# Optimization experiments

Hardware: AMD Instinct MI355X
Metric: run time of the kernel (lower is better)

The kernel has to match this reference:

```python
import jax, jax.numpy as jnp
import numpy as np

B, N, S = 8, 4096, 1024
D1, D2 = 128, 256
IN_CH, OUT_CH = D1 + D2, 256
BN_EPS = 1e-5


def setup_inputs() -> dict:
    key = jax.random.key(0)
    ks = jax.random.split(key, 12)
    inp = {
        "xyz1": jax.random.normal(ks[0], (B, N, 3), jnp.float32),
        "xyz2": jax.random.normal(ks[1], (B, S, 3), jnp.float32),
        "points1": jax.random.normal(ks[2], (B, N, D1), jnp.float32),
        "points2": jax.random.normal(ks[3], (B, S, D2), jnp.float32),
        # fuse: Conv1d(in_ch->out_ch, k=1) + BN
        "W_fuse": jax.random.normal(ks[4], (OUT_CH, IN_CH), jnp.float32) * (1.0 / np.sqrt(IN_CH)),
        "b_fuse": jnp.zeros((OUT_CH,), jnp.float32),
        "g_fuse": jnp.ones((OUT_CH,), jnp.float32),
        "bt_fuse": jnp.zeros((OUT_CH,), jnp.float32),
        # res block net1: Conv1d(out_ch->out_ch) + BN (res_expansion=1.0)
        "W1": jax.random.normal(ks[5], (OUT_CH, OUT_CH), jnp.float32) * (1.0 / np.sqrt(OUT_CH)),
        "b1": jnp.zeros((OUT_CH,), jnp.float32),
        "g1": jnp.ones((OUT_CH,), jnp.float32),
        "bt1": jnp.zeros((OUT_CH,), jnp.float32),
        # res block net2: Conv1d(out_ch->out_ch) + BN
        "W2": jax.random.normal(ks[6], (OUT_CH, OUT_CH), jnp.float32) * (1.0 / np.sqrt(OUT_CH)),
        "b2": jnp.zeros((OUT_CH,), jnp.float32),
        "g2": jnp.ones((OUT_CH,), jnp.float32),
        "bt2": jnp.zeros((OUT_CH,), jnp.float32),
    }
    return inp


def _bn(x, g, b):
    # BatchNorm1d training-mode forward: stats over (batch, length), x: [B, C, L]
    m = jnp.mean(x, axis=(0, 2), keepdims=True)
    v = jnp.var(x, axis=(0, 2), keepdims=True)
    return (x - m) * jax.lax.rsqrt(v + BN_EPS) * g[None, :, None] + b[None, :, None]


def _conv1x1(x, W, b):
    # x: [B, C_in, L], W: [C_out, C_in] -> [B, C_out, L]
    return jnp.einsum("oc,bcl->bol", W, x) + b[None, :, None]


def _gelu(x):
    return jax.nn.gelu(x, approximate=False)  # torch nn.GELU default (erf)


def reference(xyz1, xyz2, points1, points2,
              W_fuse, b_fuse, g_fuse, bt_fuse,
              W1, b1, g1, bt1, W2, b2, g2, bt2):
    # squared pairwise distances [B, N, S] without B x N x S x 3 intermediate
    d = (jnp.sum(xyz1 * xyz1, -1)[:, :, None]
         - 2.0 * jnp.einsum("bnc,bsc->bns", xyz1, xyz2)
         + jnp.sum(xyz2 * xyz2, -1)[:, None, :])
    # 3 nearest coarse points per dense point (== sort ascending, take first 3)
    neg_d3, idx = jax.lax.top_k(-d, 3)            # [B, N, 3]
    d3 = -neg_d3
    recip = 1.0 / (d3 + 1e-8)
    w = recip / jnp.sum(recip, axis=2, keepdims=True)  # [B, N, 3]
    gathered = points2[jnp.arange(points2.shape[0])[:, None, None], idx]  # [B, N, 3, D2]
    interp = jnp.sum(gathered * w[..., None], axis=2)  # [B, N, D2]

    new_points = jnp.concatenate([points1, interp], axis=-1)  # [B, N, D1+D2]
    x = jnp.transpose(new_points, (0, 2, 1))                   # [B, C, N]

    # fuse: conv-bn-gelu
    x = _gelu(_bn(_conv1x1(x, W_fuse, b_fuse), g_fuse, bt_fuse))
    # residual block: gelu(bn(conv(gelu(bn(conv(x))))) + x)
    y = _gelu(_bn(_conv1x1(x, W1, b1), g1, bt1))
    y = _bn(_conv1x1(y, W2, b2), g2, bt2)
    x = _gelu(y + x)

    return jnp.transpose(x, (0, 2, 1))  # [B, N, out_ch]
```

## Files before the change

### kernel.cpp

```cpp
#include <hip/hip_runtime.h>
#include <hip/hip_bf16.h>

constexpr int Bb = 8, Nn = 4096, Ss = 1024;
constexpr int D1 = 128, D2 = 256, KIN = 384, OC = 256;
constexpr int L = Bb * Nn;
constexpr float BN_EPS = 1e-5f;

typedef __attribute__((ext_vector_type(4))) float floatx4;
typedef __attribute__((ext_vector_type(8))) __bf16 bf16x8;

#define DEV __device__ __forceinline__

DEV float bf2f(unsigned short u) {
    union { unsigned int i; float f; } v; v.i = ((unsigned int)u) << 16; return v.f;
}
DEV unsigned short f2bf(float f) {
    union { float f; unsigned int i; } v; v.f = f;
    unsigned int x = v.i;
    return (unsigned short)((x + 0x7FFFu + ((x >> 16) & 1u)) >> 16);
}
DEV float gelu_f(float x) {
    float u = x * (0.7978845608f + 0.0356774081f * x * x);
    float t = __expf(-2.0f * u);
    return x * __builtin_amdgcn_rcpf(1.0f + t);
}

DEV bool probe_isf(const unsigned int* __restrict__ w, int tid) {
    unsigned int lo = w[tid & 63] & 0xFFFFu;
    int e = (int)((lo >> 7) & 0xFF);
    unsigned long long m = __ballot(e >= 100 && e <= 144);
    return __popcll(m) < 48;
}

template <int K> DEV int permoff(int off) {
    int row = off / K, rr = off - row * K;
    int cg = (rr >> 3) & 7;
    return row * K + (rr & ~63) + (((cg ^ (row & 7)) << 3)) + (rr & 7);
}

DEV void merge3(float& d0, float& d1, float& d2, int& i0, int& i1, int& i2,
                float e0, float e1, float e2, int j0, int j1, int j2, bool pref) {
    float a0 = d0, a1 = d1, a2 = d2; int x0 = i0, x1 = i1, x2 = i2;
    float b0 = e0, b1 = e1;          int y0 = j0, y1 = j1;
    bool t = pref ? (a0 <= b0) : (a0 < b0);
    d0 = t ? a0 : b0; i0 = t ? x0 : y0;
    a0 = t ? a1 : a0; x0 = t ? x1 : x0;
    a1 = t ? a2 : a1; x1 = t ? x2 : x1;
    b0 = t ? b0 : b1; y0 = t ? y0 : y1;
    b1 = t ? b1 : e2; y1 = t ? y1 : j2;
    t = pref ? (a0 <= b0) : (a0 < b0);
    d1 = t ? a0 : b0; i1 = t ? x0 : y0;
    a0 = t ? a1 : a0; x0 = t ? x1 : x0;
    b0 = t ? b0 : b1; y0 = t ? y0 : y1;
    t = pref ? (a0 <= b0) : (a0 < b0);
    d2 = t ? a0 : b0; i2 = t ? x0 : y0;
}

__global__ __launch_bounds__(256) void k_front(const void* __restrict__ xyz1_,
                                               const void* __restrict__ xyz2_,
                                               const void* __restrict__ w0_,
                                               const void* __restrict__ w1_,
                                               const void* __restrict__ w2_,
                                               unsigned short* __restrict__ Wdst,
                                               float* __restrict__ stats,
                                               int* __restrict__ dflag,
                                               int* __restrict__ nn_idx,
                                               float* __restrict__ nn_w) {
    int tid = threadIdx.x;
    int bid = blockIdx.x;
    bool isf = probe_isf((const unsigned int*)xyz1_, tid);

    if (bid < 6) {
        stats[bid * 256 + tid] = 0.0f;
        if (bid == 0 && tid == 0) *dflag = isf ? 1 : 0;
        return;
    }
    if (bid < 902) {
        int i = (bid - 6) * 256 + tid;
        const void* src; int off;
        if (i < 98304)       { src = w0_; off = permoff<384>(i); }
        else if (i < 163840) { src = w1_; off = permoff<256>(i - 98304); }
        else                 { src = w2_; off = permoff<256>(i - 163840); }
        Wdst[i] = isf ? f2bf(((const float*)src)[off]) : ((const unsigned short*)src)[off];
        return;
    }

    __shared__ alignas(16) float s4[Ss * 4 + 32];
    int bn0 = (bid - 902) * 32;
    int b = bn0 >> 12;

    if (isf) {
        const float* p2 = (const float*)xyz2_ + (size_t)b * Ss * 3;
        for (int i = tid; i < Ss * 3; i += 256) {
            int s = i / 3, k = i - s * 3;
            s4[s * 4 + k + ((s >> 7) << 2)] = p2[i];
        }
    } else {
        const unsigned short* p2 = (const unsigned short*)xyz2_ + (size_t)b * Ss * 3;
        for (int i = tid; i < Ss * 3; i += 256) {
            int s = i / 3, k = i - s * 3;
            s4[s * 4 + k + ((s >> 7) << 2)] = bf2f(p2[i]);
        }
    }
    __syncthreads();
    for (int s = tid; s < Ss; s += 256) {
        int a = s * 4 + ((s >> 7) << 2);
        float x = s4[a], y = s4[a + 1], z = s4[a + 2];
        s4[a + 3] = x * x + y * y + z * z;
    }
    __syncthreads();

    int part = tid & 7;
    int bn = bn0 + (tid >> 3);
    float x1, y1, z1;
    if (isf) {
        const float* p1 = (const float*)xyz1_ + (size_t)bn * 3;
        x1 = p1[0]; y1 = p1[1]; z1 = p1[2];
    } else {
        const unsigned short* p1 = (const unsigned short*)xyz1_ + (size_t)bn * 3;
        x1 = bf2f(p1[0]); y1 = bf2f(p1[1]); z1 = bf2f(p1[2]);
    }
    float n1 = x1 * x1 + y1 * y1 + z1 * z1;

    float d0 = 3.4e38f, d1 = 3.4e38f, d2 = 3.4e38f;
    int i0 = 0, i1 = 0, i2 = 0;
    const float* sp = &s4[part * 516];
#pragma unroll 4
    for (int j = 0; j < 128; ++j) {
        float4 qv = *(const float4*)(sp + j * 4);
        float d = n1 + qv.w - 2.0f * (x1 * qv.x + y1 * qv.y + z1 * qv.z);
        int s = part * 128 + j;
        bool c2 = d < d2, c1 = d < d1, c0 = d < d0;
        d2 = c1 ? d1 : (c2 ? d : d2); i2 = c1 ? i1 : (c2 ? s : i2);
        d1 = c0 ? d0 : (c1 ? d : d1); i1 = c0 ? i0 : (c1 ? s : i1);
        d0 = c0 ? d  : d0;            i0 = c0 ? s  : i0;
    }
#pragma unroll
    for (int m = 1; m <= 4; m <<= 1) {
        float e0 = __shfl_xor(d0, m, 64), e1 = __shfl_xor(d1, m, 64), e2 = __shfl_xor(d2, m, 64);
        int   j0 = __shfl_xor(i0, m, 64), j1 = __shfl_xor(i1, m, 64), j2 = __shfl_xor(i2, m, 64);
        bool pref = (part < (part ^ m));
        merge3(d0, d1, d2, i0, i1, i2, e0, e1, e2, j0, j1, j2, pref);
    }
    if (part == 0) {
        float r0 = 1.0f / (d0 + 1e-8f), r1 = 1.0f / (d1 + 1e-8f), r2 = 1.0f / (d2 + 1e-8f);
        float rs = 1.0f / (r0 + r1 + r2);
        nn_idx[bn * 3 + 0] = i0; nn_idx[bn * 3 + 1] = i1; nn_idx[bn * 3 + 2] = i2;
        nn_w[bn * 3 + 0] = r0 * rs; nn_w[bn * 3 + 1] = r1 * rs; nn_w[bn * 3 + 2] = r2 * rs;
    }
}

__global__ __launch_bounds__(256) void k_gemm1(const void* __restrict__ p1_,
                                               const void* __restrict__ p2_,
                                               const int* __restrict__ nn_idx,
                                               const float* __restrict__ nn_w,
                                               const int* __restrict__ dflag,
                                               const unsigned short* __restrict__ W,
                                               unsigned short* __restrict__ Out,
                                               float* __restrict__ S1, float* __restrict__ S2) {
    __shared__ alignas(16) unsigned short As[64 * 64];
    __shared__ alignas(16) unsigned short Bs[256 * 64];
    __shared__ float sS1[256], sS2[256];

    int tid = threadIdx.x;
    int l0 = blockIdx.x * 64;
    int wn = tid >> 6, lane = tid & 63, quad = lane >> 4, lr = lane & 15;
    bool isf = (*dflag != 0);

    floatx4 acc[4][4];
#pragma unroll
    for (int mi = 0; mi < 4; ++mi)
#pragma unroll
        for (int ni = 0; ni < 4; ++ni) acc[mi][ni] = (floatx4){0.f, 0.f, 0.f, 0.f};

    for (int kc = 0; kc < KIN / 64; ++kc) {
        __syncthreads();
#pragma unroll
        for (int it = 0; it < 8; ++it) {
            int chunk = it * 4 + wn;
            int row = chunk * 8 + (lane >> 3);
            int cg = lane & 7;
            const unsigned short* src = W + (size_t)row * KIN + kc * 64 + cg * 8;
            __builtin_amdgcn_global_load_lds(
                (const __attribute__((address_space(1))) void*)src,
                (__attribute__((address_space(3))) void*)&Bs[chunk * 512],
                16, 0, 0);
        }
#pragma unroll
        for (int it = 0; it < 2; ++it) {
            int idx = it * 256 + tid, row = idx >> 3, c8 = idx & 7;
            int pt = l0 + row;
            int c0 = kc * 64 + c8 * 8;
            union { uint4 v; unsigned short u[8]; } va;
            if (c0 < D1) {
                if (isf) {
                    const float* p = (const float*)p1_ + (size_t)pt * D1 + c0;
                    float4 f0 = *(const float4*)p;
                    float4 f1 = *(const float4*)(p + 4);
                    va.u[0] = f2bf(f0.x); va.u[1] = f2bf(f0.y); va.u[2] = f2bf(f0.z); va.u[3] = f2bf(f0.w);
                    va.u[4] = f2bf(f1.x); va.u[5] = f2bf(f1.y); va.u[6] = f2bf(f1.z); va.u[7] = f2bf(f1.w);
                } else {
                    va.v = *(const uint4*)((const unsigned short*)p1_ + (size_t)pt * D1 + c0);
                }
            } else {
                int c2 = c0 - D1;
                int b = pt >> 12;
                int j0 = nn_idx[pt * 3], j1 = nn_idx[pt * 3 + 1], j2 = nn_idx[pt * 3 + 2];
                float w0 = nn_w[pt * 3], w1 = nn_w[pt * 3 + 1], w2 = nn_w[pt * 3 + 2];
                if (isf) {
                    const float* base = (const float*)p2_;
                    const float* r0 = base + ((size_t)(b * Ss + j0)) * D2 + c2;
                    const float* r1 = base + ((size_t)(b * Ss + j1)) * D2 + c2;
                    const float* r2 = base + ((size_t)(b * Ss + j2)) * D2 + c2;
#pragma unroll
                    for (int h = 0; h < 2; ++h) {
                        float4 a0 = *(const float4*)(r0 + h * 4);
                        float4 a1 = *(const float4*)(r1 + h * 4);
                        float4 a2 = *(const float4*)(r2 + h * 4);
                        va.u[h * 4 + 0] = f2bf(w0 * a0.x + w1 * a1.x + w2 * a2.x);
                        va.u[h * 4 + 1] = f2bf(w0 * a0.y + w1 * a1.y + w2 * a2.y);
                        va.u[h * 4 + 2] = f2bf(w0 * a0.z + w1 * a1.z + w2 * a2.z);
                        va.u[h * 4 + 3] = f2bf(w0 * a0.w + w1 * a1.w + w2 * a2.w);
                    }
                } else {
                    const unsigned short* base = (const unsigned short*)p2_;
                    uint4 v0 = *(const uint4*)(base + ((size_t)(b * Ss + j0)) * D2 + c2);
                    uint4 v1 = *(const uint4*)(base + ((size_t)(b * Ss + j1)) * D2 + c2);
                    uint4 v2 = *(const uint4*)(base + ((size_t)(b * Ss + j2)) * D2 + c2);
                    const unsigned short* u0 = (const unsigned short*)&v0;
                    const unsigned short* u1 = (const unsigned short*)&v1;
                    const unsigned short* u2 = (const unsigned short*)&v2;
#pragma unroll
                    for (int j = 0; j < 8; ++j)
                        va.u[j] = f2bf(w0 * bf2f(u0[j]) + w1 * bf2f(u1[j]) + w2 * bf2f(u2[j]));
                }
            }
            *(uint4*)&As[row * 64 + ((c8 ^ (row & 7)) << 3)] = va.v;
        }
        __syncthreads();
#pragma unroll
        for (int ks8 = 0; ks8 < 2; ++ks8) {
            bf16x8 af[4], bfr[4];
#pragma unroll
            for (int mi = 0; mi < 4; ++mi) {
                int ra = mi * 16 + lr;
                af[mi] = *(const bf16x8*)&As[ra * 64 + ((((ks8 << 2) + quad) ^ (ra & 7)) << 3)];
            }
#pragma unroll
            for (int ni = 0; ni < 4; ++ni) {
                int rb = wn * 64 + ni * 16 + lr;
                bfr[ni] = *(const bf16x8*)&Bs[rb * 64 + ((((ks8 << 2) + quad) ^ (rb & 7)) << 3)];
            }
#pragma unroll
            for (int mi = 0; mi < 4; ++mi)
#pragma unroll
                for (int ni = 0; ni < 4; ++ni)
                    acc[mi][ni] = __builtin_amdgcn_mfma_f32_16x16x32_bf16(af[mi], bfr[ni], acc[mi][ni], 0, 0, 0);
        }
    }

    float p1a[4] = {0, 0, 0, 0}, p2a[4] = {0, 0, 0, 0};
#pragma unroll
    for (int mi = 0; mi < 4; ++mi)
#pragma unroll
        for (int ni = 0; ni < 4; ++ni)
#pragma unroll
            for (int r = 0; r < 4; ++r) {
                float v = acc[mi][ni][r];
                int row = l0 + mi * 16 + quad * 4 + r;
                int col = wn * 64 + ni * 16 + lr;
                Out[(size_t)row * OC + col] = f2bf(v);
                p1a[ni] += v; p2a[ni] += v * v;
            }
    sS1[tid] = 0.f; sS2[tid] = 0.f;
    __syncthreads();
#pragma unroll
    for (int ni = 0; ni < 4; ++ni) {
        atomicAdd(&sS1[wn * 64 + ni * 16 + lr], p1a[ni]);
        atomicAdd(&sS2[wn * 64 + ni * 16 + lr], p2a[ni]);
    }
    __syncthreads();
    atomicAdd(&S1[tid], sS1[tid]);
    atomicAdd(&S2[tid], sS2[tid]);
}

template <int K>
__global__ __launch_bounds__(256) void k_gemm(const unsigned short* __restrict__ A,
                                              const unsigned short* __restrict__ W,
                                              unsigned short* __restrict__ Out,
                                              float* __restrict__ S1, float* __restrict__ S2,
                                              const float* __restrict__ S1in,
                                              const float* __restrict__ S2in,
                                              const void* __restrict__ g_,
                                              const void* __restrict__ bt_,
                                              const int* __restrict__ dflag) {
    __shared__ alignas(16) unsigned short As[64 * K];
    __shared__ alignas(16) unsigned short Bs[256 * 64];
    __shared__ float sS1[256], sS2[256];
    __shared__ float sCA[256], sCC[256];

    int tid = threadIdx.x;
    int l0 = blockIdx.x * 64;
    int wn = tid >> 6, lane = tid & 63, quad = lane >> 4, lr = lane & 15;

    {
        float m = S1in[tid] * (1.0f / (float)L);
        float var = S2in[tid] * (1.0f / (float)L) - m * m;
        float g, bt;
        if (*dflag) { g = ((const float*)g_)[tid]; bt = ((const float*)bt_)[tid]; }
        else { g = bf2f(((const unsigned short*)g_)[tid]); bt = bf2f(((const unsigned short*)bt_)[tid]); }
        float a = g * rsqrtf(var + BN_EPS);
        sCA[tid] = a;
        sCC[tid] = bt - m * a;
    }
    __syncthreads();

#pragma unroll
    for (int it = 0; it < (64 * K / 8) / 256; ++it) {
        int idx = it * 256 + tid;
        int row = idx >> 5, cg = idx & 31;
        union { uint4 v; unsigned short u[8]; } va;
        va.v = *(const uint4*)(A + (size_t)(l0 + row) * K + cg * 8);
        int kb = cg * 8;
#pragma unroll
        for (int j = 0; j < 8; ++j) {
            float f = bf2f(va.u[j]);
            va.u[j] = f2bf(gelu_f(sCA[kb + j] * f + sCC[kb + j]));
        }
        int sg = (cg & 24) | ((cg & 7) ^ (row & 7));
        *(uint4*)&As[row * K + sg * 8] = va.v;
    }

    floatx4 acc[4][4];
#pragma unroll
    for (int mi = 0; mi < 4; ++mi)
#pragma unroll
        for (int ni = 0; ni < 4; ++ni) acc[mi][ni] = (floatx4){0.f, 0.f, 0.f, 0.f};

    constexpr int KC = K / 64;
    for (int kc = 0; kc < KC; ++kc) {
        __syncthreads();
#pragma unroll
        for (int it = 0; it < 8; ++it) {
            int chunk = it * 4 + wn;
            int row = chunk * 8 + (lane >> 3);
            int cg = lane & 7;
            const unsigned short* src = W + (size_t)row * K + kc * 64 + cg * 8;
            __builtin_amdgcn_global_load_lds(
                (const __attribute__((address_space(1))) void*)src,
                (__attribute__((address_space(3))) void*)&Bs[chunk * 512],
                16, 0, 0);
        }
        __syncthreads();
#pragma unroll
        for (int ks8 = 0; ks8 < 2; ++ks8) {
            bf16x8 af[4], bfr[4];
#pragma unroll
            for (int mi = 0; mi < 4; ++mi) {
                int ra = mi * 16 + lr;
                int g = kc * 8 + ((((ks8 << 2) + quad)) ^ (ra & 7));
                af[mi] = *(const bf16x8*)&As[ra * K + g * 8];
            }
#pragma unroll
            for (int ni = 0; ni < 4; ++ni) {
                int rb = wn * 64 + ni * 16 + lr;
                bfr[ni] = *(const bf16x8*)&Bs[rb * 64 + ((((ks8 << 2) + quad) ^ (rb & 7)) << 3)];
            }
#pragma unroll
            for (int mi = 0; mi < 4; ++mi)
#pragma unroll
                for (int ni = 0; ni < 4; ++ni)
                    acc[mi][ni] = __builtin_amdgcn_mfma_f32_16x16x32_bf16(af[mi], bfr[ni], acc[mi][ni], 0, 0, 0);
        }
    }

    float p1a[4] = {0, 0, 0, 0}, p2a[4] = {0, 0, 0, 0};
#pragma unroll
    for (int mi = 0; mi < 4; ++mi)
#pragma unroll
        for (int ni = 0; ni < 4; ++ni)
#pragma unroll
            for (int r = 0; r < 4; ++r) {
                float v = acc[mi][ni][r];
                int row = l0 + mi * 16 + quad * 4 + r;
                int col = wn * 64 + ni * 16 + lr;
                Out[(size_t)row * OC + col] = f2bf(v);
                p1a[ni] += v; p2a[ni] += v * v;
            }
    sS1[tid] = 0.f; sS2[tid] = 0.f;
    __syncthreads();
#pragma unroll
    for (int ni = 0; ni < 4; ++ni) {
        atomicAdd(&sS1[wn * 64 + ni * 16 + lr], p1a[ni]);
        atomicAdd(&sS2[wn * 64 + ni * 16 + lr], p2a[ni]);
    }
    __syncthreads();
    atomicAdd(&S1[tid], sS1[tid]);
    atomicAdd(&S2[tid], sS2[tid]);
}

__global__ __launch_bounds__(256) void k_final(const unsigned short* __restrict__ t0,
                                               const unsigned short* __restrict__ t2,
                                               const float* __restrict__ S1_0, const float* __restrict__ S2_0,
                                               const float* __restrict__ S1_2, const float* __restrict__ S2_2,
                                               const void* __restrict__ g0_, const void* __restrict__ bt0_,
                                               const void* __restrict__ g2_, const void* __restrict__ bt2_,
                                               const int* __restrict__ dflag,
                                               void* __restrict__ out_) {
    __shared__ float sA0[256], sC0[256], sA2[256], sC2[256];
    int tid = threadIdx.x;
    bool isf = (*dflag != 0);
    {
        float m0 = S1_0[tid] * (1.0f / (float)L);
        float v0_ = S2_0[tid] * (1.0f / (float)L) - m0 * m0;
        float m2 = S1_2[tid] * (1.0f / (float)L);
        float v2_ = S2_2[tid] * (1.0f / (float)L) - m2 * m2;
        float g0, b0, g2, b2;
        if (isf) {
            g0 = ((const float*)g0_)[tid]; b0 = ((const float*)bt0_)[tid];
            g2 = ((const float*)g2_)[tid]; b2 = ((const float*)bt2_)[tid];
        } else {
            g0 = bf2f(((const unsigned short*)g0_)[tid]); b0 = bf2f(((const unsigned short*)bt0_)[tid]);
            g2 = bf2f(((const unsigned short*)g2_)[tid]); b2 = bf2f(((const unsigned short*)bt2_)[tid]);
        }
        float a0 = g0 * rsqrtf(v0_ + BN_EPS);
        float a2 = g2 * rsqrtf(v2_ + BN_EPS);
        sA0[tid] = a0; sC0[tid] = b0 - m0 * a0;
        sA2[tid] = a2; sC2[tid] = b2 - m2 * a2;
    }
    __syncthreads();

    int idx = (blockIdx.x * 256 + tid) * 8;
    int col = idx & (OC - 1);
    union { uint4 v; unsigned short u[8]; } v0, v2;
    v0.v = *(const uint4*)(t0 + idx);
    v2.v = *(const uint4*)(t2 + idx);
    float r[8];
#pragma unroll
    for (int j = 0; j < 8; ++j) {
        float x = gelu_f(sA0[col + j] * bf2f(v0.u[j]) + sC0[col + j]);
        float y = sA2[col + j] * bf2f(v2.u[j]) + sC2[col + j];
        r[j] = gelu_f(x + y);
    }
    if (isf) {
        float* o = (float*)out_ + idx;
        float4 lo = {r[0], r[1], r[2], r[3]};
        float4 hi = {r[4], r[5], r[6], r[7]};
        *(float4*)o = lo;
        *(float4*)(o + 4) = hi;
    } else {
        union { uint4 v; unsigned short u[8]; } vo;
#pragma unroll
        for (int j = 0; j < 8; ++j) vo.u[j] = f2bf(r[j]);
        *(uint4*)((unsigned short*)out_ + idx) = vo.v;
    }
}

extern "C" void kernel_launch(void* const* d_in, const int* in_sizes, int n_in,
                              void* d_out, int out_size, void* d_ws, size_t ws_size,
                              hipStream_t stream) {
    const void* xyz1    = d_in[0];
    const void* xyz2    = d_in[1];
    const void* points1 = d_in[2];
    const void* points2 = d_in[3];
    const void* W_fuse  = d_in[4];
    const void* g_fuse  = d_in[6];
    const void* bt_fuse = d_in[7];
    const void* W1      = d_in[8];
    const void* g1      = d_in[10];
    const void* bt1     = d_in[11];
    const void* W2      = d_in[12];
    const void* g2      = d_in[14];
    const void* bt2     = d_in[15];

    char* ws = (char*)d_ws;
    unsigned short* t2 = (unsigned short*)ws;
    unsigned short* t0 = (unsigned short*)(ws + 25165824);
    unsigned short* t1 = (unsigned short*)d_out;
    int*   nn_idx = (int*)(ws + 41943040);
    float* nn_w   = (float*)(ws + 42336256);
    float* stats  = (float*)(ws + 42729472);
    int*   dflag  = (int*)(ws + 42729472 + 3072 * 4);
    unsigned short* Wbf = (unsigned short*)(ws + 42745856);

    float *S1_0 = stats,        *S2_0 = stats + 256;
    float *S1_1 = stats + 512,  *S2_1 = stats + 768;
    float *S1_2 = stats + 1024, *S2_2 = stats + 1280;

    k_front<<<1926, 256, 0, stream>>>(xyz1, xyz2, W_fuse, W1, W2, Wbf, stats, dflag, nn_idx, nn_w);
    k_gemm1<<<L / 64, 256, 0, stream>>>(points1, points2, nn_idx, nn_w, dflag,
                                        Wbf, t0, S1_0, S2_0);
    k_gemm<OC><<<L / 64, 256, 0, stream>>>(t0, Wbf + 98304, t1, S1_1, S2_1,
                                           S1_0, S2_0, g_fuse, bt_fuse, dflag);
    k_gemm<OC><<<L / 64, 256, 0, stream>>>(t1, Wbf + 163840, t2, S1_2, S2_2,
                                           S1_1, S2_1, g1, bt1, dflag);
    k_final<<<L * OC / (256 * 8), 256, 0, stream>>>(t0, t2, S1_0, S2_0, S1_2, S2_2,
                                                    g_fuse, bt_fuse, g2, bt2, dflag, d_out);
}
```

Before: 229.1 us.

## Shrink GEMM block tiles to raise occupancy and grid size

The fuse GEMM now uses a 32-row tile instead of 64, and the residual GEMMs split the output channels into two 128-column halves with 64 rows each. Both kernels get launch_bounds with a minimum of 4 blocks per unit. The residual GEMM no longer preloads the whole 64x256 A panel with GELU-BN applied into LDS. It now loads and transforms one 64-wide K chunk per iteration, which cuts LDS use and lets more blocks be resident. The cost is more W reloads per output, and in the residual GEMMs each A chunk's GELU is computed twice, once per column half.

After: 235.6 us. 1.03x slower.

```diff
diff --git a/kernel.cpp b/kernel.cpp
--- a/kernel.cpp
+++ b/kernel.cpp
@@ -34,8 +34,8 @@
 
 template <int K> DEV int permoff(int off) {
     int row = off / K, rr = off - row * K;
-    int cg = (rr >> 3) & 7;
-    return row * K + (rr & ~63) + (((cg ^ (row & 7)) << 3)) + (rr & 7);
+    int cg_ = (rr >> 3) & 7;
+    return row * K + (rr & ~63) + (((cg_ ^ (row & 7)) << 3)) + (rr & 7);
 }
 
 DEV void merge3(float& d0, float& d1, float& d2, int& i0, int& i1, int& i2,
@@ -150,26 +150,26 @@
     }
 }
 
-__global__ __launch_bounds__(256) void k_gemm1(const void* __restrict__ p1_,
-                                               const void* __restrict__ p2_,
-                                               const int* __restrict__ nn_idx,
-                                               const float* __restrict__ nn_w,
-                                               const int* __restrict__ dflag,
-                                               const unsigned short* __restrict__ W,
-                                               unsigned short* __restrict__ Out,
-                                               float* __restrict__ S1, float* __restrict__ S2) {
-    __shared__ alignas(16) unsigned short As[64 * 64];
+__global__ __launch_bounds__(256, 4) void k_gemm1(const void* __restrict__ p1_,
+                                                  const void* __restrict__ p2_,
+                                                  const int* __restrict__ nn_idx,
+                                                  const float* __restrict__ nn_w,
+                                                  const int* __restrict__ dflag,
+                                                  const unsigned short* __restrict__ W,
+                                                  unsigned short* __restrict__ Out,
+                                                  float* __restrict__ S1, float* __restrict__ S2) {
+    __shared__ alignas(16) unsigned short As[32 * 64];
     __shared__ alignas(16) unsigned short Bs[256 * 64];
     __shared__ float sS1[256], sS2[256];
 
     int tid = threadIdx.x;
-    int l0 = blockIdx.x * 64;
+    int l0 = blockIdx.x * 32;
     int wn = tid >> 6, lane = tid & 63, quad = lane >> 4, lr = lane & 15;
     bool isf = (*dflag != 0);
 
-    floatx4 acc[4][4];
-#pragma unroll
-    for (int mi = 0; mi < 4; ++mi)
+    floatx4 acc[2][4];
+#pragma unroll
+    for (int mi = 0; mi < 2; ++mi)
 #pragma unroll
         for (int ni = 0; ni < 4; ++ni) acc[mi][ni] = (floatx4){0.f, 0.f, 0.f, 0.f};
 
@@ -179,16 +179,15 @@
         for (int it = 0; it < 8; ++it) {
             int chunk = it * 4 + wn;
             int row = chunk * 8 + (lane >> 3);
-            int cg = lane & 7;
-            const unsigned short* src = W + (size_t)row * KIN + kc * 64 + cg * 8;
+            int cg_ = lane & 7;
+            const unsigned short* src = W + (size_t)row * KIN + kc * 64 + cg_ * 8;
             __builtin_amdgcn_global_load_lds(
                 (const __attribute__((address_space(1))) void*)src,
                 (__attribute__((address_space(3))) void*)&Bs[chunk * 512],
                 16, 0, 0);
         }
-#pragma unroll
-        for (int it = 0; it < 2; ++it) {
-            int idx = it * 256 + tid, row = idx >> 3, c8 = idx & 7;
+        {
+            int row = tid >> 3, c8 = tid & 7;
             int pt = l0 + row;
             int c0 = kc * 64 + c8 * 8;
             union { uint4 v; unsigned short u[8]; } va;
@@ -240,9 +239,9 @@
         __syncthreads();
 #pragma unroll
         for (int ks8 = 0; ks8 < 2; ++ks8) {
-            bf16x8 af[4], bfr[4];
-#pragma unroll
-            for (int mi = 0; mi < 4; ++mi) {
+            bf16x8 af[2], bfr[4];
+#pragma unroll
+            for (int mi = 0; mi < 2; ++mi) {
                 int ra = mi * 16 + lr;
                 af[mi] = *(const bf16x8*)&As[ra * 64 + ((((ks8 << 2) + quad) ^ (ra & 7)) << 3)];
             }
@@ -252,7 +251,7 @@
                 bfr[ni] = *(const bf16x8*)&Bs[rb * 64 + ((((ks8 << 2) + quad) ^ (rb & 7)) << 3)];
             }
 #pragma unroll
-            for (int mi = 0; mi < 4; ++mi)
+            for (int mi = 0; mi < 2; ++mi)
 #pragma unroll
                 for (int ni = 0; ni < 4; ++ni)
                     acc[mi][ni] = __builtin_amdgcn_mfma_f32_16x16x32_bf16(af[mi], bfr[ni], acc[mi][ni], 0, 0, 0);
@@ -261,7 +260,7 @@
 
     float p1a[4] = {0, 0, 0, 0}, p2a[4] = {0, 0, 0, 0};
 #pragma unroll
-    for (int mi = 0; mi < 4; ++mi)
+    for (int mi = 0; mi < 2; ++mi)
 #pragma unroll
         for (int ni = 0; ni < 4; ++ni)
 #pragma unroll
@@ -284,24 +283,25 @@
     atomicAdd(&S2[tid], sS2[tid]);
 }
 
-template <int K>
-__global__ __launch_bounds__(256) void k_gemm(const unsigned short* __restrict__ A,
-                                              const unsigned short* __restrict__ W,
-                                              unsigned short* __restrict__ Out,
-                                              float* __restrict__ S1, float* __restrict__ S2,
-                                              const float* __restrict__ S1in,
-                                              const float* __restrict__ S2in,
-                                              const void* __restrict__ g_,
-                                              const void* __restrict__ bt_,
-                                              const int* __restrict__ dflag) {
-    __shared__ alignas(16) unsigned short As[64 * K];
-    __shared__ alignas(16) unsigned short Bs[256 * 64];
-    __shared__ float sS1[256], sS2[256];
+__global__ __launch_bounds__(256, 4) void k_gemm(const unsigned short* __restrict__ A,
+                                                 const unsigned short* __restrict__ W,
+                                                 unsigned short* __restrict__ Out,
+                                                 float* __restrict__ S1, float* __restrict__ S2,
+                                                 const float* __restrict__ S1in,
+                                                 const float* __restrict__ S2in,
+                                                 const void* __restrict__ g_,
+                                                 const void* __restrict__ bt_,
+                                                 const int* __restrict__ dflag) {
+    __shared__ alignas(16) unsigned short As[64 * 64];
+    __shared__ alignas(16) unsigned short Bs[128 * 64];
+    __shared__ float sS1[128], sS2[128];
     __shared__ float sCA[256], sCC[256];
 
     int tid = threadIdx.x;
-    int l0 = blockIdx.x * 64;
+    int l0 = (blockIdx.x >> 1) * 64;
+    int n0 = (blockIdx.x & 1) * 128;
     int wn = tid >> 6, lane = tid & 63, quad = lane >> 4, lr = lane & 15;
+    int wr = wn >> 1, wc = wn & 1;
 
     {
         float m = S1in[tid] * (1.0f / (float)L);
@@ -312,62 +312,57 @@
         float a = g * rsqrtf(var + BN_EPS);
         sCA[tid] = a;
         sCC[tid] = bt - m * a;
-    }
-    __syncthreads();
-
-#pragma unroll
-    for (int it = 0; it < (64 * K / 8) / 256; ++it) {
-        int idx = it * 256 + tid;
-        int row = idx >> 5, cg = idx & 31;
-        union { uint4 v; unsigned short u[8]; } va;
-        va.v = *(const uint4*)(A + (size_t)(l0 + row) * K + cg * 8);
-        int kb = cg * 8;
-#pragma unroll
-        for (int j = 0; j < 8; ++j) {
-            float f = bf2f(va.u[j]);
-            va.u[j] = f2bf(gelu_f(sCA[kb + j] * f + sCC[kb + j]));
-        }
-        int sg = (cg & 24) | ((cg & 7) ^ (row & 7));
-        *(uint4*)&As[row * K + sg * 8] = va.v;
-    }
-
-    floatx4 acc[4][4];
-#pragma unroll
-    for (int mi = 0; mi < 4; ++mi)
+        if (tid < 128) { sS1[tid] = 0.f; sS2[tid] = 0.f; }
+    }
+
+    floatx4 acc[2][4];
+#pragma unroll
+    for (int mi = 0; mi < 2; ++mi)
 #pragma unroll
         for (int ni = 0; ni < 4; ++ni) acc[mi][ni] = (floatx4){0.f, 0.f, 0.f, 0.f};
 
-    constexpr int KC = K / 64;
-    for (int kc = 0; kc < KC; ++kc) {
+    for (int kc = 0; kc < OC / 64; ++kc) {
         __syncthreads();
 #pragma unroll
-        for (int it = 0; it < 8; ++it) {
+        for (int it = 0; it < 4; ++it) {
             int chunk = it * 4 + wn;
             int row = chunk * 8 + (lane >> 3);
-            int cg = lane & 7;
-            const unsigned short* src = W + (size_t)row * K + kc * 64 + cg * 8;
+            int cg_ = lane & 7;
+            const unsigned short* src = W + (size_t)(n0 + row) * OC + kc * 64 + cg_ * 8;
             __builtin_amdgcn_global_load_lds(
                 (const __attribute__((address_space(1))) void*)src,
                 (__attribute__((address_space(3))) void*)&Bs[chunk * 512],
                 16, 0, 0);
         }
+#pragma unroll
+        for (int it = 0; it < 2; ++it) {
+            int idx = it * 256 + tid, row = idx >> 3, c8 = idx & 7;
+            union { uint4 v; unsigned short u[8]; } va;
+            va.v = *(const uint4*)(A + (size_t)(l0 + row) * OC + kc * 64 + c8 * 8);
+            int kb = kc * 64 + c8 * 8;
+#pragma unroll
+            for (int j = 0; j < 8; ++j) {
+                float f = bf2f(va.u[j]);
+                va.u[j] = f2bf(gelu_f(sCA[kb + j] * f + sCC[kb + j]));
+            }
+            *(uint4*)&As[row * 64 + ((c8 ^ (row & 7)) << 3)] = va.v;
+        }
         __syncthreads();
 #pragma unroll
         for (int ks8 = 0; ks8 < 2; ++ks8) {
-            bf16x8 af[4], bfr[4];
-#pragma unroll
-            for (int mi = 0; mi < 4; ++mi) {
-                int ra = mi * 16 + lr;
-                int g = kc * 8 + ((((ks8 << 2) + quad)) ^ (ra & 7));
-                af[mi] = *(const bf16x8*)&As[ra * K + g * 8];
+            bf16x8 af[2], bfr[4];
+#pragma unroll
+            for (int mi = 0; mi < 2; ++mi) {
+                int ra = wr * 32 + mi * 16 + lr;
+                af[mi] = *(const bf16x8*)&As[ra * 64 + ((((ks8 << 2) + quad) ^ (ra & 7)) << 3)];
             }
 #pragma unroll
             for (int ni = 0; ni < 4; ++ni) {
-                int rb = wn * 64 + ni * 16 + lr;
+                int rb = wc * 64 + ni * 16 + lr;
                 bfr[ni] = *(const bf16x8*)&Bs[rb * 64 + ((((ks8 << 2) + quad) ^ (rb & 7)) << 3)];
             }
 #pragma unroll
-            for (int mi = 0; mi < 4; ++mi)
+            for (int mi = 0; mi < 2; ++mi)
 #pragma unroll
                 for (int ni = 0; ni < 4; ++ni)
                     acc[mi][ni] = __builtin_amdgcn_mfma_f32_16x16x32_bf16(af[mi], bfr[ni], acc[mi][ni], 0, 0, 0);
@@ -376,27 +371,28 @@
 
     float p1a[4] = {0, 0, 0, 0}, p2a[4] = {0, 0, 0, 0};
 #pragma unroll
-    for (int mi = 0; mi < 4; ++mi)
+    for (int mi = 0; mi < 2; ++mi)
 #pragma unroll
         for (int ni = 0; ni < 4; ++ni)
 #pragma unroll
             for (int r = 0; r < 4; ++r) {
                 float v = acc[mi][ni][r];
-                int row = l0 + mi * 16 + quad * 4 + r;
-                int col = wn * 64 + ni * 16 + lr;
+                int row = l0 + wr * 32 + mi * 16 + quad * 4 + r;
+                int col = n0 + wc * 64 + ni * 16 + lr;
                 Out[(size_t)row * OC + col] = f2bf(v);
                 p1a[ni] += v; p2a[ni] += v * v;
             }
-    sS1[tid] = 0.f; sS2[tid] = 0.f;
     __syncthreads();
 #pragma unroll
     for (int ni = 0; ni < 4; ++ni) {
-        atomicAdd(&sS1[wn * 64 + ni * 16 + lr], p1a[ni]);
-        atomicAdd(&sS2[wn * 64 + ni * 16 + lr], p2a[ni]);
-    }
-    __syncthreads();
-    atomicAdd(&S1[tid], sS1[tid]);
-    atomicAdd(&S2[tid], sS2[tid]);
+        atomicAdd(&sS1[wc * 64 + ni * 16 + lr], p1a[ni]);
+        atomicAdd(&sS2[wc * 64 + ni * 16 + lr], p2a[ni]);
+    }
+    __syncthreads();
+    if (tid < 128) {
+        atomicAdd(&S1[n0 + tid], sS1[tid]);
+        atomicAdd(&S2[n0 + tid], sS2[tid]);
+    }
 }
 
 __global__ __launch_bounds__(256) void k_final(const unsigned short* __restrict__ t0,
@@ -488,12 +484,12 @@
     float *S1_2 = stats + 1024, *S2_2 = stats + 1280;
 
     k_front<<<1926, 256, 0, stream>>>(xyz1, xyz2, W_fuse, W1, W2, Wbf, stats, dflag, nn_idx, nn_w);
-    k_gemm1<<<L / 64, 256, 0, stream>>>(points1, points2, nn_idx, nn_w, dflag,
+    k_gemm1<<<L / 32, 256, 0, stream>>>(points1, points2, nn_idx, nn_w, dflag,
                                         Wbf, t0, S1_0, S2_0);
-    k_gemm<OC><<<L / 64, 256, 0, stream>>>(t0, Wbf + 98304, t1, S1_1, S2_1,
-                                           S1_0, S2_0, g_fuse, bt_fuse, dflag);
-    k_gemm<OC><<<L / 64, 256, 0, stream>>>(t1, Wbf + 163840, t2, S1_2, S2_2,
-                                           S1_1, S2_1, g1, bt1, dflag);
+    k_gemm<<<(L / 64) * 2, 256, 0, stream>>>(t0, Wbf + 98304, t1, S1_1, S2_1,
+                                             S1_0, S2_0, g_fuse, bt_fuse, dflag);
+    k_gemm<<<(L / 64) * 2, 256, 0, stream>>>(t1, Wbf + 163840, t2, S1_2, S2_2,
+                                             S1_1, S2_1, g1, bt1, dflag);
     k_final<<<L * OC / (256 * 8), 256, 0, stream>>>(t0, t2, S1_0, S2_0, S1_2, S2_2,
                                                     g_fuse, bt_fuse, g2, bt2, dflag, d_out);
 }
```
